# Kernel tuning notes

Measured on AMD Instinct MI355X. Metric: run time of the kernel, lower is better.

The kernel has to match this reference:

```python
import jax, jax.numpy as jnp
import numpy as np

EPS_GN = 1e-8
EPS_ATTN = 1e-8


def setup_inputs() -> dict:
    key = jax.random.key(0)
    ks = jax.random.split(key, 13)
    B, C, N = 4, 512, 2048
    s = 0.02
    return {
        "x": jax.random.normal(ks[0], (B, C, N), jnp.float32),
        "dw_w": jax.random.normal(ks[1], (C, 3), jnp.float32) * s,
        "pw_w": jax.random.normal(ks[2], (C, C), jnp.float32) * s,
        "u_w": jax.random.normal(ks[3], (2 * C, C), jnp.float32) * s,
        "u_b": jax.random.normal(ks[4], (2 * C,), jnp.float32) * s,
        "v_w": jax.random.normal(ks[5], (2 * C, C), jnp.float32) * s,
        "v_b": jax.random.normal(ks[6], (2 * C,), jnp.float32) * s,
        "h_w": jax.random.normal(ks[7], (C, C), jnp.float32) * s,
        "h_b": jax.random.normal(ks[8], (C,), jnp.float32) * s,
        "q_w": jax.random.normal(ks[9], (C, C), jnp.float32) * s,
        "k_w": jax.random.normal(ks[10], (C, C), jnp.float32) * s,
        "o_w": jax.random.normal(ks[11], (C, 2 * C), jnp.float32) * s,
        "o_b": jax.random.normal(ks[12], (C,), jnp.float32) * s,
    }


def reference(x, dw_w, pw_w, u_w, u_b, v_w, v_b, h_w, h_b, q_w, k_w, o_w, o_b):
    # x: [B, C, N]
    C = x.shape[1]
    # GroupNorm(1, C): normalize over (C, N) per sample; affine is identity-init
    # in torch but we follow the module math with default weight=1, bias=0
    mean = jnp.mean(x, axis=(1, 2), keepdims=True)
    var = jnp.var(x, axis=(1, 2), keepdims=True)
    z = (x - mean) * jax.lax.rsqrt(var + EPS_GN)

    # local depthwise conv k=3, pad=1 (cross-correlation), no bias
    zp = jnp.pad(z, ((0, 0), (0, 0), (1, 1)))
    dw = (dw_w[:, 0, None] * zp[:, :, :-2]
          + dw_w[:, 1, None] * zp[:, :, 1:-1]
          + dw_w[:, 2, None] * zp[:, :, 2:])
    # pointwise conv (no bias)
    z = z + jnp.einsum('oc,bcn->bon', pw_w, dw)

    u = jax.nn.sigmoid(jnp.einsum('oc,bcn->bon', u_w, z) + u_b[:, None])  # [B,2C,N]
    v = jnp.einsum('oc,bcn->bon', v_w, z) + v_b[:, None]                  # [B,2C,N]
    h = jnp.einsum('oc,bcn->bno', h_w, z) + h_b                           # [B,N,C]

    q = h @ q_w.T  # [B,N,C]
    k = h @ k_w.T  # [B,N,C]
    scale = 1.0 / jnp.sqrt(jnp.float32(C))

    logits = jnp.einsum('bnc,bmc->bnm', q, k) * scale
    a = jax.nn.relu(logits)
    a = a * a
    a = a / (jnp.sum(a, axis=-1, keepdims=True) + EPS_ATTN)

    av = jnp.einsum('bnm,bom->bon', a, v)  # [B,2C,N]
    y = jnp.einsum('oc,bcn->bon', o_w, u * av) + o_b[:, None]
    return x + y
```

## Files before the change

kernel.cpp:

```cpp
#include <hip/hip_runtime.h>
#include <hip/hip_bf16.h>
#include <cstdint>

typedef __bf16 bhalf;
typedef __bf16 bhalf8 __attribute__((ext_vector_type(8)));
typedef float f32x4 __attribute__((ext_vector_type(4)));

enum { EPI_Z2=0, EPI_UV=1, EPI_BIAS=2, EPI_QK=3, EPI_ATTN=4, EPI_PV=5, EPI_Y=6 };

__device__ __forceinline__ void gl_lds16(const bhalf* g, bhalf* l) {
  __builtin_amdgcn_global_load_lds(
      (const __attribute__((address_space(1))) unsigned int*)g,
      (__attribute__((address_space(3))) unsigned int*)l,
      16, 0, 0);
}
__device__ __forceinline__ void barrier_raw() { asm volatile("s_barrier" ::: "memory"); }
#define VMW(n)  asm volatile("s_waitcnt vmcnt(" #n ")" ::: "memory")
#define LGKM0() asm volatile("s_waitcnt lgkmcnt(0)" ::: "memory")


template<int EPI>
__global__ void __launch_bounds__(512, 2)
g8n(const bhalf* __restrict__ A, const bhalf* __restrict__ Bw,
    void* __restrict__ Out, void* __restrict__ Out2,
    const bhalf* __restrict__ auxb, const float* __restrict__ auxf,
    int N, int K, long sB, float scale, int rowshift)
{
  constexpr int STRIDE = 384*64;
  __shared__ __align__(16) char lds[3*STRIDE];

  const int gx = gridDim.x, gy = gridDim.y;
  const int nwg = gx*gy;
  const int flat = blockIdx.y*gx + blockIdx.x;
  const int q8 = nwg>>3, r8 = nwg&7, xcd = flat&7, o8 = flat>>3;
  const int wsw = (xcd<r8 ? xcd*(q8+1) : r8*(q8+1)+(xcd-r8)*q8) + o8;
  const int bx = wsw % gx, by = wsw / gx;
  const int m0 = by*256, n0 = bx*128;

  const bhalf* Ab = A;
  const bhalf* Bb = Bw + (rowshift ? (long)(m0>>rowshift)*sB : 0);

  const int tid = threadIdx.x, wid = tid>>6, lane = tid&63;
  const int lm = lane&15, kq = lane>>4;
  const int wm = wid>>1, wn = wid&1;
  const int srow = lane>>2;
  const int csw = ((lane&3) ^ ((lane>>3)&3)) * 8;
  const int kqs = kq ^ ((lm>>1)&3);

  f32x4 acc[4][4];
  #pragma unroll
  for (int i=0;i<4;i++)
    #pragma unroll
    for (int j=0;j<4;j++) acc[i][j] = f32x4{0.f,0.f,0.f,0.f};

  auto stage = [&](int buf, int t){
    char* base = lds + buf*STRIDE;
    const int k0 = t*32;
    #pragma unroll
    for (int c=0;c<3;c++){
      const int r0 = wid*48 + c*16;
      bhalf* d = (bhalf*)(base + r0*64);
      const bhalf* g = (r0 < 256)
        ? Ab + (long)(m0 + r0 + srow)*K + k0 + csw
        : Bb + (long)(n0 + r0 - 256 + srow)*K + k0 + csw;
      gl_lds16(g, d);
    }
  };

  auto compute = [&](int buf){
    char* base = lds + buf*STRIDE;
    bhalf8 af[4], bf[4];
    #pragma unroll
    for (int i=0;i<4;i++)
      af[i] = *(const bhalf8*)(base + (wm*64 + i*16 + lm)*64 + kqs*16);
    #pragma unroll
    for (int j=0;j<4;j++)
      bf[j] = *(const bhalf8*)(base + (256 + wn*64 + j*16 + lm)*64 + kqs*16);
    __builtin_amdgcn_s_setprio(1);
    #pragma unroll
    for (int i=0;i<4;i++)
      #pragma unroll
      for (int j=0;j<4;j++)
        acc[i][j] = __builtin_amdgcn_mfma_f32_16x16x32_bf16(af[i], bf[j], acc[i][j], 0,0,0);
    __builtin_amdgcn_s_setprio(0);
  };

  const int NT = K>>5;
  stage(0,0); stage(1,1);
  int b0 = 0;
  for (int t=0; t<NT; ++t){
    if (t+2<NT){
      int b2 = b0+2; if (b2>=3) b2-=3;
      stage(b2, t+2);
      VMW(6);
    } else if (t+1<NT) { VMW(3); }
    else               { VMW(0); }
    barrier_raw();
    compute(b0);
    barrier_raw();
    if (++b0==3) b0=0;
  }

  char* obase; int ldb;
  if constexpr (EPI==EPI_PV){
    obase = (char*)Out + 2*((long)m0*1024 + n0); ldb = 2048;
  }
  if constexpr (EPI==EPI_QK){
    bool qh = n0 < 512;
    obase = (char*)(qh?Out:Out2) + 2*((long)m0*512 + (n0 - (qh?0:512)));
    ldb = 1024;
  }
  #pragma unroll
  for (int i=0;i<4;i++){
    #pragma unroll
    for (int j=0;j<4;j++){
      const int lcol = wn*64 + j*16 + lm;
      #pragma unroll
      for (int r=0;r<4;r++){
        const int lrow = wm*64 + i*16 + kq*4 + r;
        float v = acc[i][j][r];
        if constexpr (EPI==EPI_PV){
          const int rowg = m0 + lrow;
          float den = auxf[rowg];
          v *= __builtin_amdgcn_rcpf(den + 1e-8f);
          v *= (float)auxb[(long)rowg*1024 + n0 + lcol];
        }
        const int cb = lcol*2;
        const int lb = lrow*256 + (((cb>>5) ^ ((lrow>>2)&3))<<5) + (cb&31);
        *(bhalf*)(lds + lb) = (bhalf)v;
      }
    }
  }
  LGKM0();
  barrier_raw();
  #pragma unroll
  for (int it=0; it<8; ++it){
    const int g = (it*512 + tid)*16;
    const int row = g >> 8, off = g & 255;
    const int lb = row*256 + (((off>>5) ^ ((row>>2)&3))<<5) + (off&31);
    uint4 val = *(const uint4*)(lds + lb);
    *(uint4*)(obase + (long)row*ldb + off) = val;
  }
  (void)scale; (void)auxb; (void)auxf; (void)N;
}

template<int EPI>
__global__ void __launch_bounds__(512, 2)
g8(const bhalf* __restrict__ A, const bhalf* __restrict__ Bw,
   void* __restrict__ Out, void* __restrict__ Out2,
   const float* __restrict__ bias, const float* __restrict__ bias2,
   int N, int K, long sA, long sB, long sO, long sAuxf, float scale)
{
  constexpr int ASL = 256*64;
  constexpr int ABUF = 2*ASL;
  constexpr int STRIDE = 2*ABUF;
  __shared__ __align__(16) char lds[2*STRIDE];

  const int gx = gridDim.x, gy = gridDim.y;
  const int nwg = gx*gy;
  const int flat = blockIdx.y*gx + blockIdx.x;
  const int q8 = nwg>>3, r8 = nwg&7, xcd = flat&7, o8 = flat>>3;
  const int wsw = (xcd<r8 ? xcd*(q8+1) : r8*(q8+1)+(xcd-r8)*q8) + o8;
  const int bx = wsw % gx, by = wsw / gx;
  const int m0 = by*256, n0 = bx*256;
  const int bz = blockIdx.z;

  const bhalf* Ab = A + (long)bz*sA;
  const bhalf* Bb = Bw + (long)bz*sB;

  const int tid = threadIdx.x, wid = tid>>6, lane = tid&63;
  const int lm = lane&15, kq = lane>>4;
  const int wm = wid>>2, wn = wid&3;
  const int srow = lane>>2;
  const int csw = ((lane&3) ^ ((lane>>3)&3)) * 8;
  const int kqs = kq ^ ((lm>>1)&3);

  f32x4 acc[8][4];
  #pragma unroll
  for (int i=0;i<8;i++)
    #pragma unroll
    for (int j=0;j<4;j++) acc[i][j] = f32x4{0.f,0.f,0.f,0.f};

  auto stage = [&](int buf, int t){
    char* base = lds + buf*STRIDE;
    const int k0 = t*64;
    #pragma unroll
    for (int ksl=0; ksl<2; ksl++){
      #pragma unroll
      for (int c=0;c<2;c++){
        bhalf* dA = (bhalf*)(base + ksl*ASL + (wid*32 + c*16)*64);
        gl_lds16(Ab + (long)(m0 + wid*32 + c*16 + srow)*K + k0 + ksl*32 + csw, dA);
        bhalf* dB = (bhalf*)(base + ABUF + ksl*ASL + (wid*32 + c*16)*64);
        gl_lds16(Bb + (long)(n0 + wid*32 + c*16 + srow)*K + k0 + ksl*32 + csw, dB);
      }
    }
  };

  auto compute = [&](int buf){
    char* base = lds + buf*STRIDE;
    #pragma unroll
    for (int ks=0; ks<2; ks++){
      bhalf8 af[8], bf[4];
      #pragma unroll
      for (int i=0;i<8;i++)
        af[i] = *(const bhalf8*)(base + ks*ASL + (wm*128 + i*16 + lm)*64 + kqs*16);
      #pragma unroll
      for (int j=0;j<4;j++)
        bf[j] = *(const bhalf8*)(base + ABUF + ks*ASL + (wn*64 + j*16 + lm)*64 + kqs*16);
      __builtin_amdgcn_s_setprio(1);
      #pragma unroll
      for (int i=0;i<8;i++)
        #pragma unroll
        for (int j=0;j<4;j++)
          acc[i][j] = __builtin_amdgcn_mfma_f32_16x16x32_bf16(af[i], bf[j], acc[i][j], 0,0,0);
      __builtin_amdgcn_s_setprio(0);
    }
  };

  const int NT = K>>6;
  stage(0,0);
  for (int t=0; t<NT; ++t){
    if (t+1<NT){ stage((t+1)&1, t+1); VMW(8); }
    else       { VMW(0); }
    barrier_raw();
    compute(t&1);
    barrier_raw();
  }

  char* obase; int ldb;
  const float* bv = nullptr; int bc0 = 0; bool sig = false;
  if constexpr (EPI==EPI_ATTN){
    obase = (char*)Out + 2*((long)bz*sO + (long)m0*N + n0); ldb = N*2;
  }
  if constexpr (EPI==EPI_UV){
    bool uh = n0 < 1024; sig = uh;
    obase = (char*)(uh?Out:Out2) + 2*((long)m0*1024 + (n0 - (uh?0:1024)));
    ldb = 2048; bv = uh ? bias : bias2; bc0 = uh ? n0 : n0-1024;
  }

  float rs[8][4];
  if constexpr (EPI==EPI_ATTN){
    #pragma unroll
    for (int i=0;i<8;i++)
      #pragma unroll
      for (int r=0;r<4;r++) rs[i][r]=0.f;
  }
  #pragma unroll
  for (int i=0;i<8;i++){
    #pragma unroll
    for (int j=0;j<4;j++){
      const int lcol = wn*64 + j*16 + lm;
      #pragma unroll
      for (int r=0;r<4;r++){
        const int lrow = wm*128 + i*16 + kq*4 + r;
        float v = acc[i][j][r];
        if constexpr (EPI==EPI_ATTN){
          v *= scale; v = fmaxf(v,0.f); v = v*v;
          rs[i][r] += v;
        }
        if constexpr (EPI==EPI_UV){
          v += bv[bc0 + lcol];
          if (sig) v = 1.f/(1.f + __expf(-v));
        }
        const int cb = lcol*2;
        const int lb = lrow*512 + (((cb>>5) ^ ((lrow>>2)&3))<<5) + (cb&31);
        *(bhalf*)(lds + lb) = (bhalf)v;
      }
    }
  }
  if constexpr (EPI==EPI_ATTN){
    float* rd = (float*)Out2;
    #pragma unroll
    for (int i=0;i<8;i++){
      const int rbase = m0 + wm*128 + i*16 + kq*4;
      #pragma unroll
      for (int r=0;r<4;r++){
        float s = rs[i][r];
        s += __shfl_xor(s,1); s += __shfl_xor(s,2);
        s += __shfl_xor(s,4); s += __shfl_xor(s,8);
        if (lm==0) atomicAdd(rd + (long)bz*sAuxf + rbase + r, s);
      }
    }
  }
  LGKM0();
  barrier_raw();
  #pragma unroll
  for (int it=0; it<16; ++it){
    const int g = (it*512 + tid)*16;
    const int row = g >> 9, off = g & 511;
    const int lb = row*512 + (((off>>5) ^ ((row>>2)&3))<<5) + (off&31);
    uint4 val = *(const uint4*)(lds + lb);
    *(uint4*)(obase + (long)row*ldb + off) = val;
  }
  (void)scale; (void)bias; (void)bias2; (void)N;
}

template<int EPI>
__global__ void __launch_bounds__(512, 2)
gemm_bt(const bhalf* __restrict__ A, const bhalf* __restrict__ Bw,
        void* __restrict__ Out,
        const float* __restrict__ bias,
        const bhalf* __restrict__ auxb,
        int M, int N, int K)
{
  constexpr int STRIDE = 256*64;
  __shared__ __align__(16) char lds[4*STRIDE];

  const int gx = gridDim.x, gy = gridDim.y;
  const int nwg = gx*gy;
  const int flat = blockIdx.y*gx + blockIdx.x;
  const int q8 = nwg>>3, r8 = nwg&7, xcd = flat&7, o8 = flat>>3;
  const int w = (xcd<r8 ? xcd*(q8+1) : r8*(q8+1)+(xcd-r8)*q8) + o8;
  const int bx = w % gx, by = w / gx;

  const int tid = threadIdx.x;
  const int wid = tid>>6, lane = tid&63;
  const int lm = lane&15, kq = lane>>4;
  const int wm = wid>>2, wn = wid&3;
  const int m0 = by*128, n0 = bx*128;
  const int srow = lane>>2;
  const int csw = ((lane&3) ^ ((lane>>3)&3))*8;
  const int kqs = kq ^ ((lm>>1)&3);

  f32x4 acc[4][2];
  #pragma unroll
  for (int i=0;i<4;i++)
    #pragma unroll
    for (int j=0;j<2;j++) acc[i][j] = f32x4{0.f,0.f,0.f,0.f};

  auto stage = [&](int t){
    char* base = lds + (t&3)*STRIDE;
    const int k0 = t*32;
    #pragma unroll
    for (int c=0;c<2;c++){
      const int r0 = wid*32 + c*16;
      bhalf* d = (bhalf*)(base + r0*64);
      const bhalf* g = (r0 < 128)
        ? A + (long)(m0 + r0 + srow)*K + k0 + csw
        : Bw + (long)(n0 + r0 - 128 + srow)*K + k0 + csw;
      gl_lds16(g, d);
    }
  };

  auto compute = [&](int t){
    char* base = lds + (t&3)*STRIDE;
    bhalf8 af[4], bf[2];
    #pragma unroll
    for (int i=0;i<4;i++)
      af[i] = *(const bhalf8*)(base + (wm*64 + i*16 + lm)*64 + kqs*16);
    #pragma unroll
    for (int j=0;j<2;j++)
      bf[j] = *(const bhalf8*)(base + (128 + wn*32 + j*16 + lm)*64 + kqs*16);
    __builtin_amdgcn_s_setprio(1);
    #pragma unroll
    for (int i=0;i<4;i++)
      #pragma unroll
      for (int j=0;j<2;j++)
        acc[i][j] = __builtin_amdgcn_mfma_f32_16x16x32_bf16(af[i], bf[j], acc[i][j], 0,0,0);
    __builtin_amdgcn_s_setprio(0);
  };

  const int NT = K>>5;
  stage(0); stage(1); stage(2);
  for (int t=0; t<NT; ++t){
    if (t+3<NT){ stage(t+3); VMW(6); }
    else if (t+2<NT) { VMW(4); }
    else if (t+1<NT) { VMW(2); }
    else             { VMW(0); }
    barrier_raw();
    compute(t);
    barrier_raw();
  }

  char* obase = (char*)Out + 2*((long)m0*N + n0);
  const int ldb = N*2;
  #pragma unroll
  for (int i=0;i<4;i++){
    #pragma unroll
    for (int j=0;j<2;j++){
      const int lcol = wn*32 + j*16 + lm;
      #pragma unroll
      for (int r=0;r<4;r++){
        const int lrow = wm*64 + i*16 + kq*4 + r;
        float v = acc[i][j][r];
        if constexpr (EPI==EPI_Z2)
          v += (float)auxb[(long)(m0+lrow)*N + n0 + lcol];
        if constexpr (EPI==EPI_BIAS || EPI==EPI_Y)
          v += bias[n0 + lcol];
        const int cb = lcol*2;
        const int lb = lrow*256 + (((cb>>5) ^ ((lrow>>2)&3))<<5) + (cb&31);
        *(bhalf*)(lds + lb) = (bhalf)v;
      }
    }
  }
  LGKM0();
  barrier_raw();
  #pragma unroll
  for (int it=0; it<4; ++it){
    const int g = (it*512 + tid)*16;
    const int row = g >> 8, off = g & 255;
    const int lb = row*256 + (((off>>5) ^ ((row>>2)&3))<<5) + (off&31);
    uint4 val = *(const uint4*)(lds + lb);
    *(uint4*)(obase + (long)row*ldb + off) = val;
  }
  (void)M;
}

struct CvtArgs { const float* src[7]; bhalf* dst[7]; int n[7]; };
__global__ void cvt_multi(CvtArgs a) {
  int seg = blockIdx.y;
  int i = (blockIdx.x*256 + threadIdx.x)*4;
  if (i >= a.n[seg]) return;
  float4 f = *(const float4*)(a.src[seg] + i);
  bhalf* d = a.dst[seg] + i;
  d[0]=(bhalf)f.x; d[1]=(bhalf)f.y; d[2]=(bhalf)f.z; d[3]=(bhalf)f.w;
}

__global__ void gn_part(const float* __restrict__ x, float* __restrict__ ps, float* __restrict__ pss) {
  int b = blockIdx.y;
  const float* xb = x + (long)b*(512*2048);
  float s=0.f, ss=0.f;
  #pragma unroll
  for (int it=0; it<8; it++){
    int idx = ((it*128 + blockIdx.x)*256 + threadIdx.x)*4;
    float4 f = *(const float4*)(xb + idx);
    s  += f.x+f.y+f.z+f.w;
    ss += f.x*f.x+f.y*f.y+f.z*f.z+f.w*f.w;
  }
  for (int off=32; off; off>>=1){ s += __shfl_xor(s,off); ss += __shfl_xor(ss,off); }
  __shared__ float ls[4], lss[4];
  int wid = threadIdx.x>>6, lane = threadIdx.x&63;
  if (lane==0){ ls[wid]=s; lss[wid]=ss; }
  __syncthreads();
  if (threadIdx.x==0){
    s = ls[0]+ls[1]+ls[2]+ls[3]; ss = lss[0]+lss[1]+lss[2]+lss[3];
    ps[b*128 + blockIdx.x] = s; pss[b*128 + blockIdx.x] = ss;
  }
}

__global__ void gn_final(const float* __restrict__ ps, const float* __restrict__ pss,
                         float* __restrict__ stats) {
  int b = blockIdx.x;
  float s = ps[b*128 + threadIdx.x], ss = pss[b*128 + threadIdx.x];
  for (int off=32; off; off>>=1){ s += __shfl_xor(s,off); ss += __shfl_xor(ss,off); }
  __shared__ float l0[2], l1[2];
  int wid = threadIdx.x>>6, lane = threadIdx.x&63;
  if (lane==0){ l0[wid]=s; l1[wid]=ss; }
  __syncthreads();
  if (threadIdx.x==0){
    s = l0[0]+l0[1]; ss = l1[0]+l1[1];
    float mean = s*(1.f/1048576.f);
    float var  = ss*(1.f/1048576.f) - mean*mean;
    stats[b*2] = mean; stats[b*2+1] = rsqrtf(var + 1e-8f);
  }
}

__global__ void norm_dw_T(const float* __restrict__ x, const float* __restrict__ stats,
                          const float* __restrict__ dw_w,
                          bhalf* __restrict__ zT, bhalf* __restrict__ dwT) {
  int b = blockIdx.z, n0 = blockIdx.x*32, c0 = blockIdx.y*32;
  float mean = stats[b*2], rstd = stats[b*2+1];
  __shared__ float zs[32][35];
  int tx = threadIdx.x, ty = threadIdx.y;
  #pragma unroll
  for (int r=0;r<4;r++){
    int c = c0 + ty + r*8;
    for (int cc=tx; cc<34; cc+=32){
      int n = n0 - 1 + cc;
      float v = 0.f;
      if (n>=0 && n<2048) v = (x[((long)b*512 + c)*2048 + n] - mean)*rstd;
      zs[ty + r*8][cc] = v;
    }
  }
  __syncthreads();
  float w0 = dw_w[(c0+tx)*3+0], w1 = dw_w[(c0+tx)*3+1], w2 = dw_w[(c0+tx)*3+2];
  #pragma unroll
  for (int r=0;r<4;r++){
    int ln = ty + r*8;
    float z = zs[tx][ln+1];
    float d = w0*zs[tx][ln] + w1*zs[tx][ln+1] + w2*zs[tx][ln+2];
    long o = ((long)b*2048 + n0 + ln)*512 + c0 + tx;
    zT[o] = (bhalf)z; dwT[o] = (bhalf)d;
  }
}

__global__ void transpose_bf16(const bhalf* __restrict__ in, bhalf* __restrict__ out,
                               int R, int C) {
  __shared__ bhalf t[32][33];
  int r0 = blockIdx.x*32, c0 = blockIdx.y*32;
  long ib = (long)blockIdx.z*R*C;
  int tx = threadIdx.x, ty = threadIdx.y;
  #pragma unroll
  for (int r=0;r<4;r++)
    t[ty + r*8][tx] = in[ib + (long)(r0 + ty + r*8)*C + c0 + tx];
  __syncthreads();
  #pragma unroll
  for (int r=0;r<4;r++)
    out[ib + (long)(c0 + ty + r*8)*R + r0 + tx] = t[tx][ty + r*8];
}

__global__ void final_add(const float* __restrict__ x, const bhalf* __restrict__ yT,
                          float* __restrict__ out) {
  __shared__ float t[32][33];
  int n0 = blockIdx.x*32, c0 = blockIdx.y*32, b = blockIdx.z;
  int tx = threadIdx.x, ty = threadIdx.y;
  #pragma unroll
  for (int r=0;r<4;r++)
    t[ty + r*8][tx] = (float)yT[((long)b*2048 + n0 + ty + r*8)*512 + c0 + tx];
  __syncthreads();
  #pragma unroll
  for (int r=0;r<4;r++){
    long idx = ((long)b*512 + c0 + ty + r*8)*2048 + n0 + tx;
    out[idx] = x[idx] + t[tx][ty + r*8];
  }
}

extern "C" void kernel_launch(void* const* d_in, const int* in_sizes, int n_in,
                              void* d_out, int out_size, void* d_ws, size_t ws_size,
                              hipStream_t stream) {
  (void)in_sizes; (void)n_in; (void)out_size; (void)ws_size;
  const float* x    = (const float*)d_in[0];
  const float* dw_w = (const float*)d_in[1];
  const float* pw_w = (const float*)d_in[2];
  const float* u_w  = (const float*)d_in[3];
  const float* u_b  = (const float*)d_in[4];
  const float* v_w  = (const float*)d_in[5];
  const float* v_b  = (const float*)d_in[6];
  const float* h_w  = (const float*)d_in[7];
  const float* h_b  = (const float*)d_in[8];
  const float* q_w  = (const float*)d_in[9];
  const float* k_w  = (const float*)d_in[10];
  const float* o_w  = (const float*)d_in[11];
  const float* o_b  = (const float*)d_in[12];
  float* out = (float*)d_out;

  char* ws = (char*)d_ws;
  size_t off = 0;
  auto alloc = [&](size_t bytes) -> void* {
    void* p = ws + off; off = (off + bytes + 255) & ~(size_t)255; return p;
  };

  float* ps    = (float*)alloc(4*128*4);
  float* pss   = (float*)alloc(4*128*4);
  float* stats = (float*)alloc(4*2*4);
  float* rden  = (float*)alloc(4*2048*4);
  bhalf* wb_pw = (bhalf*)alloc(512*512*2);
  bhalf* wb_uv = (bhalf*)alloc((size_t)2048*512*2);
  bhalf* wb_h  = (bhalf*)alloc(512*512*2);
  bhalf* wb_qk = (bhalf*)alloc((size_t)1024*512*2);
  bhalf* wb_o  = (bhalf*)alloc((size_t)512*1024*2);
  const size_t ACT = (size_t)4*2048*512;
  bhalf* zT   = (bhalf*)alloc(ACT*2);
  bhalf* dwT  = (bhalf*)alloc(ACT*2);
  bhalf* z2T  = (bhalf*)alloc(ACT*2);
  bhalf* ub   = (bhalf*)alloc(ACT*2*2);
  bhalf* vT   = (bhalf*)alloc(ACT*2*2);
  bhalf* v_fm = (bhalf*)alloc(ACT*2*2);
  bhalf* hb   = (bhalf*)alloc(ACT*2);
  bhalf* wsc  = (bhalf*)alloc((size_t)4*2048*2048*2);
  bhalf* uav  = (bhalf*)alloc(ACT*2*2);
  bhalf* qb = zT;  bhalf* kb = dwT;  bhalf* yT = vT;

  hipMemsetAsync(rden, 0, 4*2048*4, stream);

  CvtArgs ca;
  ca.src[0]=pw_w; ca.dst[0]=wb_pw;           ca.n[0]=512*512;
  ca.src[1]=u_w;  ca.dst[1]=wb_uv;           ca.n[1]=1024*512;
  ca.src[2]=v_w;  ca.dst[2]=wb_uv+1024*512;  ca.n[2]=1024*512;
  ca.src[3]=h_w;  ca.dst[3]=wb_h;            ca.n[3]=512*512;
  ca.src[4]=q_w;  ca.dst[4]=wb_qk;           ca.n[4]=512*512;
  ca.src[5]=k_w;  ca.dst[5]=wb_qk+512*512;   ca.n[5]=512*512;
  ca.src[6]=o_w;  ca.dst[6]=wb_o;            ca.n[6]=512*1024;
  cvt_multi<<<dim3(512,7), 256, 0, stream>>>(ca);

  gn_part<<<dim3(128,4), 256, 0, stream>>>(x, ps, pss);
  gn_final<<<dim3(4), 128, 0, stream>>>(ps, pss, stats);

  norm_dw_T<<<dim3(64,16,4), dim3(32,8), 0, stream>>>(x, stats, dw_w, zT, dwT);

  const float iscl = 0.044194173824159216f;
  gemm_bt<EPI_Z2><<<dim3(4,64,1), 512, 0, stream>>>(dwT, wb_pw, z2T,
      nullptr, zT, 8192, 512, 512);
  g8<EPI_UV><<<dim3(8,32,1), 512, 0, stream>>>(z2T, wb_uv, ub, vT,
      u_b, v_b, 2048, 512, 0, 0, 0, 0, 0.f);
  gemm_bt<EPI_BIAS><<<dim3(4,64,1), 512, 0, stream>>>(z2T, wb_h, hb,
      h_b, nullptr, 8192, 512, 512);
  g8n<EPI_QK><<<dim3(8,32,1), 512, 0, stream>>>(hb, wb_qk, qb, kb,
      nullptr, nullptr, 1024, 512, 0, 0.f, 0);
  transpose_bf16<<<dim3(64,32,4), dim3(32,8), 0, stream>>>(vT, v_fm, 2048, 1024);
  g8<EPI_ATTN><<<dim3(8,8,4), 512, 0, stream>>>(qb, kb, wsc, rden,
      nullptr, nullptr, 2048, 512,
      (long)2048*512, (long)2048*512, (long)2048*2048, 2048, iscl);
  g8n<EPI_PV><<<dim3(8,32,1), 512, 0, stream>>>(wsc, v_fm, uav, nullptr,
      ub, rden, 1024, 2048, (long)1024*2048, 0.f, 11);
  gemm_bt<EPI_Y><<<dim3(4,64,1), 512, 0, stream>>>(uav, wb_o, yT,
      o_b, nullptr, 8192, 512, 1024);
  final_add<<<dim3(64,16,4), dim3(32,8), 0, stream>>>(x, yT, out);
}
```

Baseline: 202.0 us.

## Split GEMM main loops into interleaved LDS-read/MFMA quarter phases with staggered staging

Restructures the 256x256 (gA) and 256x128 (gB) bf16 GEMM kernels so each K-tile is consumed in quarter or half phases. Each phase reads part of the A/B fragments from LDS and issues 16 MFMAs, and global-to-LDS staging of the A and B halves is staggered between phases. gB now uses 64-wide K tiles with triple buffering instead of 32-wide. The goal is to overlap LDS reads and global loads with MFMA work and to cut per-tile barrier overhead, at the cost of more barriers per tile and more LDS (gB uses about 144KB).

New measurement: 192.3 us. 4.8% less time.

```diff
diff --git a/kernel.cpp b/kernel.cpp
--- a/kernel.cpp
+++ b/kernel.cpp
@@ -21,140 +21,15 @@
 
 template<int EPI>
 __global__ void __launch_bounds__(512, 2)
-g8n(const bhalf* __restrict__ A, const bhalf* __restrict__ Bw,
-    void* __restrict__ Out, void* __restrict__ Out2,
-    const bhalf* __restrict__ auxb, const float* __restrict__ auxf,
-    int N, int K, long sB, float scale, int rowshift)
-{
-  constexpr int STRIDE = 384*64;
-  __shared__ __align__(16) char lds[3*STRIDE];
-
-  const int gx = gridDim.x, gy = gridDim.y;
-  const int nwg = gx*gy;
-  const int flat = blockIdx.y*gx + blockIdx.x;
-  const int q8 = nwg>>3, r8 = nwg&7, xcd = flat&7, o8 = flat>>3;
-  const int wsw = (xcd<r8 ? xcd*(q8+1) : r8*(q8+1)+(xcd-r8)*q8) + o8;
-  const int bx = wsw % gx, by = wsw / gx;
-  const int m0 = by*256, n0 = bx*128;
-
-  const bhalf* Ab = A;
-  const bhalf* Bb = Bw + (rowshift ? (long)(m0>>rowshift)*sB : 0);
-
-  const int tid = threadIdx.x, wid = tid>>6, lane = tid&63;
-  const int lm = lane&15, kq = lane>>4;
-  const int wm = wid>>1, wn = wid&1;
-  const int srow = lane>>2;
-  const int csw = ((lane&3) ^ ((lane>>3)&3)) * 8;
-  const int kqs = kq ^ ((lm>>1)&3);
-
-  f32x4 acc[4][4];
-  #pragma unroll
-  for (int i=0;i<4;i++)
-    #pragma unroll
-    for (int j=0;j<4;j++) acc[i][j] = f32x4{0.f,0.f,0.f,0.f};
-
-  auto stage = [&](int buf, int t){
-    char* base = lds + buf*STRIDE;
-    const int k0 = t*32;
-    #pragma unroll
-    for (int c=0;c<3;c++){
-      const int r0 = wid*48 + c*16;
-      bhalf* d = (bhalf*)(base + r0*64);
-      const bhalf* g = (r0 < 256)
-        ? Ab + (long)(m0 + r0 + srow)*K + k0 + csw
-        : Bb + (long)(n0 + r0 - 256 + srow)*K + k0 + csw;
-      gl_lds16(g, d);
-    }
-  };
-
-  auto compute = [&](int buf){
-    char* base = lds + buf*STRIDE;
-    bhalf8 af[4], bf[4];
-    #pragma unroll
-    for (int i=0;i<4;i++)
-      af[i] = *(const bhalf8*)(base + (wm*64 + i*16 + lm)*64 + kqs*16);
-    #pragma unroll
-    for (int j=0;j<4;j++)
-      bf[j] = *(const bhalf8*)(base + (256 + wn*64 + j*16 + lm)*64 + kqs*16);
-    __builtin_amdgcn_s_setprio(1);
-    #pragma unroll
-    for (int i=0;i<4;i++)
-      #pragma unroll
-      for (int j=0;j<4;j++)
-        acc[i][j] = __builtin_amdgcn_mfma_f32_16x16x32_bf16(af[i], bf[j], acc[i][j], 0,0,0);
-    __builtin_amdgcn_s_setprio(0);
-  };
-
-  const int NT = K>>5;
-  stage(0,0); stage(1,1);
-  int b0 = 0;
-  for (int t=0; t<NT; ++t){
-    if (t+2<NT){
-      int b2 = b0+2; if (b2>=3) b2-=3;
-      stage(b2, t+2);
-      VMW(6);
-    } else if (t+1<NT) { VMW(3); }
-    else               { VMW(0); }
-    barrier_raw();
-    compute(b0);
-    barrier_raw();
-    if (++b0==3) b0=0;
-  }
-
-  char* obase; int ldb;
-  if constexpr (EPI==EPI_PV){
-    obase = (char*)Out + 2*((long)m0*1024 + n0); ldb = 2048;
-  }
-  if constexpr (EPI==EPI_QK){
-    bool qh = n0 < 512;
-    obase = (char*)(qh?Out:Out2) + 2*((long)m0*512 + (n0 - (qh?0:512)));
-    ldb = 1024;
-  }
-  #pragma unroll
-  for (int i=0;i<4;i++){
-    #pragma unroll
-    for (int j=0;j<4;j++){
-      const int lcol = wn*64 + j*16 + lm;
-      #pragma unroll
-      for (int r=0;r<4;r++){
-        const int lrow = wm*64 + i*16 + kq*4 + r;
-        float v = acc[i][j][r];
-        if constexpr (EPI==EPI_PV){
-          const int rowg = m0 + lrow;
-          float den = auxf[rowg];
-          v *= __builtin_amdgcn_rcpf(den + 1e-8f);
-          v *= (float)auxb[(long)rowg*1024 + n0 + lcol];
-        }
-        const int cb = lcol*2;
-        const int lb = lrow*256 + (((cb>>5) ^ ((lrow>>2)&3))<<5) + (cb&31);
-        *(bhalf*)(lds + lb) = (bhalf)v;
-      }
-    }
-  }
-  LGKM0();
-  barrier_raw();
-  #pragma unroll
-  for (int it=0; it<8; ++it){
-    const int g = (it*512 + tid)*16;
-    const int row = g >> 8, off = g & 255;
-    const int lb = row*256 + (((off>>5) ^ ((row>>2)&3))<<5) + (off&31);
-    uint4 val = *(const uint4*)(lds + lb);
-    *(uint4*)(obase + (long)row*ldb + off) = val;
-  }
-  (void)scale; (void)auxb; (void)auxf; (void)N;
-}
-
-template<int EPI>
-__global__ void __launch_bounds__(512, 2)
-g8(const bhalf* __restrict__ A, const bhalf* __restrict__ Bw,
+gA(const bhalf* __restrict__ A, const bhalf* __restrict__ Bw,
    void* __restrict__ Out, void* __restrict__ Out2,
    const float* __restrict__ bias, const float* __restrict__ bias2,
    int N, int K, long sA, long sB, long sO, long sAuxf, float scale)
 {
-  constexpr int ASL = 256*64;
-  constexpr int ABUF = 2*ASL;
-  constexpr int STRIDE = 2*ABUF;
-  __shared__ __align__(16) char lds[2*STRIDE];
+  constexpr int KSL = 256*64;
+  constexpr int REG = 2*KSL;
+  constexpr int DBUF = 2*REG;
+  __shared__ __align__(16) char lds[2*DBUF];
 
   const int gx = gridDim.x, gy = gridDim.y;
   const int nwg = gx*gy;
@@ -181,51 +56,78 @@
     #pragma unroll
     for (int j=0;j<4;j++) acc[i][j] = f32x4{0.f,0.f,0.f,0.f};
 
-  auto stage = [&](int buf, int t){
-    char* base = lds + buf*STRIDE;
-    const int k0 = t*64;
-    #pragma unroll
-    for (int ksl=0; ksl<2; ksl++){
-      #pragma unroll
-      for (int c=0;c<2;c++){
-        bhalf* dA = (bhalf*)(base + ksl*ASL + (wid*32 + c*16)*64);
-        gl_lds16(Ab + (long)(m0 + wid*32 + c*16 + srow)*K + k0 + ksl*32 + csw, dA);
-        bhalf* dB = (bhalf*)(base + ABUF + ksl*ASL + (wid*32 + c*16)*64);
-        gl_lds16(Bb + (long)(n0 + wid*32 + c*16 + srow)*K + k0 + ksl*32 + csw, dB);
+  auto stageA = [&](int kt){
+    char* base = lds + (kt&1)*DBUF;
+    const int k0 = kt*64;
+    #pragma unroll
+    for (int h=0; h<2; h++)
+      #pragma unroll
+      for (int ksl=0; ksl<2; ksl++){
+        bhalf* d = (bhalf*)(base + ksl*KSL + (h*128 + wid*16)*64);
+        gl_lds16(Ab + (long)(m0 + h*128 + wid*16 + srow)*K + k0 + ksl*32 + csw, d);
       }
-    }
-  };
-
-  auto compute = [&](int buf){
-    char* base = lds + buf*STRIDE;
-    #pragma unroll
-    for (int ks=0; ks<2; ks++){
-      bhalf8 af[8], bf[4];
-      #pragma unroll
-      for (int i=0;i<8;i++)
-        af[i] = *(const bhalf8*)(base + ks*ASL + (wm*128 + i*16 + lm)*64 + kqs*16);
-      #pragma unroll
-      for (int j=0;j<4;j++)
-        bf[j] = *(const bhalf8*)(base + ABUF + ks*ASL + (wn*64 + j*16 + lm)*64 + kqs*16);
-      __builtin_amdgcn_s_setprio(1);
-      #pragma unroll
-      for (int i=0;i<8;i++)
+  };
+  auto stageB = [&](int kt){
+    char* base = lds + (kt&1)*DBUF + REG;
+    const int k0 = kt*64;
+    #pragma unroll
+    for (int h=0; h<2; h++)
+      #pragma unroll
+      for (int ksl=0; ksl<2; ksl++){
+        bhalf* d = (bhalf*)(base + ksl*KSL + (h*128 + wid*16)*64);
+        gl_lds16(Bb + (long)(n0 + h*128 + wid*16 + srow)*K + k0 + ksl*32 + csw, d);
+      }
+  };
+
+  bhalf8 af[4][2], bf[4][2];
+  auto readA = [&](int kt, int ih){
+    char* base = lds + (kt&1)*DBUF;
+    #pragma unroll
+    for (int i2=0;i2<4;i2++)
+      #pragma unroll
+      for (int ksl=0;ksl<2;ksl++)
+        af[i2][ksl] = *(const bhalf8*)(base + ksl*KSL + (wm*128 + ih*64 + i2*16 + lm)*64 + kqs*16);
+  };
+  auto readB = [&](int kt, int jh){
+    char* base = lds + (kt&1)*DBUF + REG;
+    #pragma unroll
+    for (int j2=0;j2<2;j2++)
+      #pragma unroll
+      for (int ksl=0;ksl<2;ksl++)
+        bf[jh*2+j2][ksl] = *(const bhalf8*)(base + ksl*KSL + (wn*64 + jh*32 + j2*16 + lm)*64 + kqs*16);
+  };
+  auto mfma16 = [&](int ih, int jh){
+    __builtin_amdgcn_s_setprio(1);
+    #pragma unroll
+    for (int i2=0;i2<4;i2++)
+      #pragma unroll
+      for (int j2=0;j2<2;j2++)
         #pragma unroll
-        for (int j=0;j<4;j++)
-          acc[i][j] = __builtin_amdgcn_mfma_f32_16x16x32_bf16(af[i], bf[j], acc[i][j], 0,0,0);
-      __builtin_amdgcn_s_setprio(0);
-    }
+        for (int ksl=0;ksl<2;ksl++)
+          acc[ih*4+i2][jh*2+j2] = __builtin_amdgcn_mfma_f32_16x16x32_bf16(
+              af[i2][ksl], bf[jh*2+j2][ksl], acc[ih*4+i2][jh*2+j2], 0,0,0);
+    __builtin_amdgcn_s_setprio(0);
   };
 
   const int NT = K>>6;
-  stage(0,0);
-  for (int t=0; t<NT; ++t){
-    if (t+1<NT){ stage((t+1)&1, t+1); VMW(8); }
-    else       { VMW(0); }
-    barrier_raw();
-    compute(t&1);
-    barrier_raw();
-  }
+  stageA(0); stageB(0); stageA(1);
+  for (int kt=0; kt<NT; ++kt){
+    if (kt==NT-1) { VMW(0); } else { VMW(4); }
+    barrier_raw();
+    readA(kt,0); readB(kt,0);
+    if (kt+1<NT) stageB(kt+1);
+    mfma16(0,0);
+    barrier_raw();
+    readB(kt,1);
+    mfma16(0,1);
+    barrier_raw();
+    readA(kt,1);
+    mfma16(1,0);
+    barrier_raw();
+    if (kt+2<NT) stageA(kt+2);
+    mfma16(1,1);
+  }
+  barrier_raw();
 
   char* obase; int ldb;
   const float* bv = nullptr; int bc0 = 0; bool sig = false;
@@ -293,6 +195,147 @@
     *(uint4*)(obase + (long)row*ldb + off) = val;
   }
   (void)scale; (void)bias; (void)bias2; (void)N;
+}
+
+template<int EPI>
+__global__ void __launch_bounds__(512, 2)
+gB(const bhalf* __restrict__ A, const bhalf* __restrict__ Bw,
+   void* __restrict__ Out, void* __restrict__ Out2,
+   const bhalf* __restrict__ auxb, const float* __restrict__ auxf,
+   int N, int K, long sB, float scale, int rowshift)
+{
+  constexpr int KSLA = 256*64;
+  constexpr int KSLB = 128*64;
+  constexpr int REGA = 2*KSLA;
+  constexpr int DBUF = REGA + 2*KSLB;
+  __shared__ __align__(16) char lds[3*DBUF];
+
+  const int gx = gridDim.x, gy = gridDim.y;
+  const int nwg = gx*gy;
+  const int flat = blockIdx.y*gx + blockIdx.x;
+  const int q8 = nwg>>3, r8 = nwg&7, xcd = flat&7, o8 = flat>>3;
+  const int wsw = (xcd<r8 ? xcd*(q8+1) : r8*(q8+1)+(xcd-r8)*q8) + o8;
+  const int bx = wsw % gx, by = wsw / gx;
+  const int m0 = by*256, n0 = bx*128;
+
+  const bhalf* Ab = A;
+  const bhalf* Bb = Bw + (rowshift ? (long)(m0>>rowshift)*sB : 0);
+
+  const int tid = threadIdx.x, wid = tid>>6, lane = tid&63;
+  const int lm = lane&15, kq = lane>>4;
+  const int wm = wid>>1, wn = wid&1;
+  const int srow = lane>>2;
+  const int csw = ((lane&3) ^ ((lane>>3)&3)) * 8;
+  const int kqs = kq ^ ((lm>>1)&3);
+
+  f32x4 acc[4][4];
+  #pragma unroll
+  for (int i=0;i<4;i++)
+    #pragma unroll
+    for (int j=0;j<4;j++) acc[i][j] = f32x4{0.f,0.f,0.f,0.f};
+
+  auto stageAB = [&](int kt){
+    char* base = lds + (kt%3)*DBUF;
+    const int k0 = kt*64;
+    #pragma unroll
+    for (int h=0; h<2; h++)
+      #pragma unroll
+      for (int ksl=0; ksl<2; ksl++){
+        bhalf* d = (bhalf*)(base + ksl*KSLA + (h*128 + wid*16)*64);
+        gl_lds16(Ab + (long)(m0 + h*128 + wid*16 + srow)*K + k0 + ksl*32 + csw, d);
+      }
+    #pragma unroll
+    for (int ksl=0; ksl<2; ksl++){
+      bhalf* d = (bhalf*)(base + REGA + ksl*KSLB + (wid*16)*64);
+      gl_lds16(Bb + (long)(n0 + wid*16 + srow)*K + k0 + ksl*32 + csw, d);
+    }
+  };
+
+  bhalf8 af[4][2], bf[4][2];
+  auto readA = [&](int kt){
+    char* base = lds + (kt%3)*DBUF;
+    #pragma unroll
+    for (int i2=0;i2<4;i2++)
+      #pragma unroll
+      for (int ksl=0;ksl<2;ksl++)
+        af[i2][ksl] = *(const bhalf8*)(base + ksl*KSLA + (wm*64 + i2*16 + lm)*64 + kqs*16);
+  };
+  auto readB = [&](int kt, int jh){
+    char* base = lds + (kt%3)*DBUF + REGA;
+    #pragma unroll
+    for (int j2=0;j2<2;j2++)
+      #pragma unroll
+      for (int ksl=0;ksl<2;ksl++)
+        bf[jh*2+j2][ksl] = *(const bhalf8*)(base + ksl*KSLB + (wn*64 + jh*32 + j2*16 + lm)*64 + kqs*16);
+  };
+  auto mfma16 = [&](int jh){
+    __builtin_amdgcn_s_setprio(1);
+    #pragma unroll
+    for (int i2=0;i2<4;i2++)
+      #pragma unroll
+      for (int j2=0;j2<2;j2++)
+        #pragma unroll
+        for (int ksl=0;ksl<2;ksl++)
+          acc[i2][jh*2+j2] = __builtin_amdgcn_mfma_f32_16x16x32_bf16(
+              af[i2][ksl], bf[jh*2+j2][ksl], acc[i2][jh*2+j2], 0,0,0);
+    __builtin_amdgcn_s_setprio(0);
+  };
+
+  const int NT = K>>6;
+  stageAB(0); stageAB(1);
+  for (int kt=0; kt<NT; ++kt){
+    if (kt==NT-1) { VMW(0); } else { VMW(6); }
+    barrier_raw();
+    readA(kt); readB(kt,0);
+    if (kt+2<NT) stageAB(kt+2);
+    mfma16(0);
+    barrier_raw();
+    readB(kt,1);
+    mfma16(1);
+  }
+  barrier_raw();
+
+  char* obase; int ldb;
+  if constexpr (EPI==EPI_PV){
+    obase = (char*)Out + 2*((long)m0*1024 + n0); ldb = 2048;
+  }
+  if constexpr (EPI==EPI_QK){
+    bool qh = n0 < 512;
+    obase = (char*)(qh?Out:Out2) + 2*((long)m0*512 + (n0 - (qh?0:512)));
+    ldb = 1024;
+  }
+  #pragma unroll
+  for (int i=0;i<4;i++){
+    #pragma unroll
+    for (int j=0;j<4;j++){
+      const int lcol = wn*64 + j*16 + lm;
+      #pragma unroll
+      for (int r=0;r<4;r++){
+        const int lrow = wm*64 + i*16 + kq*4 + r;
+        float v = acc[i][j][r];
+        if constexpr (EPI==EPI_PV){
+          const int rowg = m0 + lrow;
+          float den = auxf[rowg];
+          v *= __builtin_amdgcn_rcpf(den + 1e-8f);
+          v *= (float)auxb[(long)rowg*1024 + n0 + lcol];
+        }
+        const int cb = lcol*2;
+        const int lb = lrow*256 + (((cb>>5) ^ ((lrow>>2)&3))<<5) + (cb&31);
+        *(bhalf*)(lds + lb) = (bhalf)v;
+      }
+    }
+  }
+  LGKM0();
+  barrier_raw();
+  #pragma unroll
+  for (int it=0; it<8; ++it){
+    const int g = (it*512 + tid)*16;
+    const int row = g >> 8, off = g & 255;
+    const int lb = row*256 + (((off>>5) ^ ((row>>2)&3))<<5) + (off&31);
+    uint4 val = *(const uint4*)(lds + lb);
+    *(uint4*)(obase + (long)row*ldb + off) = val;
+  }
+  (void)scale; (void)auxb; (void)auxf; (void)N;
 }
 
 template<int EPI>
@@ -581,17 +624,17 @@
   const float iscl = 0.044194173824159216f;
   gemm_bt<EPI_Z2><<<dim3(4,64,1), 512, 0, stream>>>(dwT, wb_pw, z2T,
       nullptr, zT, 8192, 512, 512);
-  g8<EPI_UV><<<dim3(8,32,1), 512, 0, stream>>>(z2T, wb_uv, ub, vT,
+  gA<EPI_UV><<<dim3(8,32,1), 512, 0, stream>>>(z2T, wb_uv, ub, vT,
       u_b, v_b, 2048, 512, 0, 0, 0, 0, 0.f);
   gemm_bt<EPI_BIAS><<<dim3(4,64,1), 512, 0, stream>>>(z2T, wb_h, hb,
       h_b, nullptr, 8192, 512, 512);
-  g8n<EPI_QK><<<dim3(8,32,1), 512, 0, stream>>>(hb, wb_qk, qb, kb,
+  gB<EPI_QK><<<dim3(8,32,1), 512, 0, stream>>>(hb, wb_qk, qb, kb,
       nullptr, nullptr, 1024, 512, 0, 0.f, 0);
   transpose_bf16<<<dim3(64,32,4), dim3(32,8), 0, stream>>>(vT, v_fm, 2048, 1024);
-  g8<EPI_ATTN><<<dim3(8,8,4), 512, 0, stream>>>(qb, kb, wsc, rden,
+  gA<EPI_ATTN><<<dim3(8,8,4), 512, 0, stream>>>(qb, kb, wsc, rden,
       nullptr, nullptr, 2048, 512,
       (long)2048*512, (long)2048*512, (long)2048*2048, 2048, iscl);
-  g8n<EPI_PV><<<dim3(8,32,1), 512, 0, stream>>>(wsc, v_fm, uav, nullptr,
+  gB<EPI_PV><<<dim3(8,32,1), 512, 0, stream>>>(wsc, v_fm, uav, nullptr,
       ub, rden, 1024, 2048, (long)1024*2048, 0.f, 11);
   gemm_bt<EPI_Y><<<dim3(4,64,1), 512, 0, stream>>>(uav, wb_o, yT,
       o_b, nullptr, 8192, 512, 1024);
```
